# Performance work log

Hardware: AMD Instinct MI355X
Metric: run time of the kernel (lower is better)

Reference implementation:

```python
import jax, jax.numpy as jnp
import numpy as np

N_NODES = 250000
N_EDGES = 4000000
N_GRAPHS = 512
NEG_SLOPE = 0.01  # F.leaky_relu default


def _glorot(key, shape):
    fan_in, fan_out = shape
    lim = (6.0 / (fan_in + fan_out)) ** 0.5
    return jax.random.uniform(key, shape, jnp.float32, -lim, lim)


def setup_inputs() -> dict:
    key = jax.random.key(0)
    ks = jax.random.split(key, 12)
    x = jax.random.normal(ks[0], (N_NODES, 13), jnp.float32)
    edge_index = jax.random.randint(ks[1], (2, N_EDGES), 0, N_NODES, jnp.int64)
    batch_index = jnp.sort(jax.random.randint(ks[2], (N_NODES,), 0, N_GRAPHS, jnp.int64))
    # SAGEConv params: lin_l (neighbor agg, with bias), lin_r (self, no bias)
    dims = [(13, 16), (16, 8), (8, 4)]
    params = {}
    for i, (di, do) in enumerate(dims, 1):
        params[f'W{i}l'] = _glorot(ks[2 + 2 * i], (di, do))
        params[f'b{i}'] = jnp.zeros((do,), jnp.float32)
        params[f'W{i}r'] = _glorot(ks[3 + 2 * i], (di, do))
    params['Wc'] = _glorot(ks[10], (8, 1))
    params['bc'] = jnp.zeros((1,), jnp.float32)
    return dict(x=x, edge_index=edge_index, batch_index=batch_index, **params)


def _sage_conv(x, src, dst, Wl, bl, Wr):
    # mean-aggregate neighbor features at target nodes, then linear
    msg_sum = jax.ops.segment_sum(x[src], dst, num_segments=N_NODES)  # [N, d]
    cnt = jax.ops.segment_sum(jnp.ones((src.shape[0],), x.dtype), dst,
                              num_segments=N_NODES)
    agg = msg_sum / jnp.maximum(cnt, 1.0)[:, None]
    return agg @ Wl + bl + x @ Wr


def reference(x, edge_index, batch_index,
              W1l, b1, W1r, W2l, b2, W2r, W3l, b3, W3r, Wc, bc):
    src, dst = edge_index[0], edge_index[1]
    h = jax.nn.leaky_relu(_sage_conv(x, src, dst, W1l, b1, W1r), NEG_SLOPE)
    h = jax.nn.leaky_relu(_sage_conv(h, src, dst, W2l, b2, W2r), NEG_SLOPE)
    h = _sage_conv(h, src, dst, W3l, b3, W3r)  # [N, 4]
    add_pool = jax.ops.segment_sum(h, batch_index, num_segments=N_GRAPHS)  # [G,4]
    gcnt = jax.ops.segment_sum(jnp.ones((N_NODES,), h.dtype), batch_index,
                               num_segments=N_GRAPHS)
    mean_pool = add_pool / jnp.maximum(gcnt, 1.0)[:, None]
    g = jnp.concatenate([mean_pool, add_pool], axis=1)  # [G, 8]
    return g @ Wc + bc  # [G, 1]
```

## Files before the change

kernel.cpp:

```cpp
#include <hip/hip_runtime.h>

#define N_NODES 250000
#define N_EDGES 4000000
#define N_GRAPHS 512
#define NEG 0.01f
#define BINB 9
#define WIN 512
#define NBINS 489
#define NSUB (NBINS * 4)
#define CAPQ 2560
#define PART_EPB 8192
#define PART_BLOCKS 489
#define PACK_BLOCKS 1954

__device__ __forceinline__ float lrelu(float v) { return v > 0.0f ? v : NEG * v; }
__device__ __forceinline__ unsigned f2b(float f) {
    unsigned u = __float_as_uint(f);
    unsigned r = ((u >> 16) & 1u) + 0x7FFFu;
    return (u + r) >> 16;
}
__device__ __forceinline__ unsigned pk(float a, float b) { return f2b(a) | (f2b(b) << 16); }
__device__ __forceinline__ float blo(unsigned p) { return __uint_as_float(p << 16); }
__device__ __forceinline__ float bhi(unsigned p) { return __uint_as_float(p & 0xFFFF0000u); }

__global__ __launch_bounds__(1024) void part_pack_k(const int* __restrict__ src,
                                                    const int* __restrict__ dst,
                                                    int* __restrict__ qcnt,
                                                    unsigned* __restrict__ binned,
                                                    const float* __restrict__ x,
                                                    unsigned* __restrict__ x16b) {
    if (blockIdx.x >= PART_BLOCKS) {
        int tid = (blockIdx.x - PART_BLOCKS) * 1024 + threadIdx.x;
        if (tid < N_NODES * 8) {
            int n = tid >> 3, d2 = tid & 7;
            int a = d2 * 2, b = a + 1;
            float va = (a < 13) ? x[n * 13 + a] : 0.0f;
            float vb = (b < 13) ? x[n * 13 + b] : 0.0f;
            x16b[tid] = pk(va, vb);
        }
        return;
    }
    __shared__ int hist[NSUB];
    __shared__ int loff[NSUB];
    __shared__ int base[NSUB];
    __shared__ unsigned ebuf[PART_EPB];
    __shared__ unsigned short subid[PART_EPB];
    __shared__ int wsum[16];
    int t = threadIdx.x;
    for (int i = t; i < NSUB; i += 1024) hist[i] = 0;
    __syncthreads();
    unsigned e0 = blockIdx.x * PART_EPB;
    int m = min((int)PART_EPB, (int)(N_EDGES - e0));
    for (int i = t; i < m; i += 1024) {
        unsigned e = e0 + i;
        int s = ((dst[e] >> BINB) << 2) | (src[e] >> 16);
        atomicAdd(&hist[s], 1);
    }
    __syncthreads();
    int p = 0, s0 = 0, incl = 0;
    if (t < NSUB / 2) { s0 = hist[2 * t]; p = s0 + hist[2 * t + 1]; }
    incl = p;
#pragma unroll
    for (int d = 1; d < 64; d <<= 1) {
        int u = __shfl_up(incl, d, 64);
        if ((t & 63) >= d) incl += u;
    }
    if ((t & 63) == 63) wsum[t >> 6] = incl;
    __syncthreads();
    if (t == 0) {
        int r = 0;
#pragma unroll
        for (int i = 0; i < 16; i++) { int s = wsum[i]; wsum[i] = r; r += s; }
    }
    __syncthreads();
    if (t < NSUB / 2) {
        int ex = incl + wsum[t >> 6] - p;
        loff[2 * t] = ex;
        loff[2 * t + 1] = ex + s0;
    }
    __syncthreads();
    for (int i = t; i < NSUB; i += 1024) {
        int h = hist[i];
        base[i] = (h > 0) ? atomicAdd(&qcnt[i], h) : 0;
    }
    __syncthreads();
    for (int i = t; i < NSUB; i += 1024) hist[i] = loff[i];
    __syncthreads();
    for (int i = t; i < m; i += 1024) {
        unsigned e = e0 + i;
        int d = dst[e], sv = src[e];
        int s = ((d >> BINB) << 2) | (sv >> 16);
        int pos = atomicAdd(&hist[s], 1);
        ebuf[pos] = ((unsigned)(d & (WIN - 1)) << 18) | (unsigned)sv;
        subid[pos] = (unsigned short)s;
    }
    __syncthreads();
    for (int j = t; j < m; j += 1024) {
        int s = subid[j];
        binned[(size_t)s * CAPQ + base[s] + (j - loff[s])] = ebuf[j];
    }
}

__global__ __launch_bounds__(1024) void sortagg_k(const unsigned* __restrict__ x16b,
                                                  unsigned* __restrict__ binned,
                                                  const int* __restrict__ qcnt,
                                                  int* __restrict__ offs,
                                                  float* __restrict__ cntf,
                                                  float* __restrict__ agg) {
    __shared__ unsigned stg[CAPQ];
    __shared__ unsigned srt[CAPQ];
    __shared__ int hist[WIN];
    __shared__ int cur[WIN];
    __shared__ int wsum[8];
    int t = threadIdx.x;
    int bin = blockIdx.x;
    int f = t & (WIN - 1), l = t >> 9;
    int lane = t & 63, wv = t >> 6;
    float a0 = 0, a1 = 0, a2 = 0, a3 = 0, a4 = 0, a5 = 0, a6 = 0, a7 = 0;
    int deg = 0;
    for (int q = 0; q < 4; q++) {
        int sub = (bin << 2) | q;
        int cnt = qcnt[sub];
        unsigned* bp = binned + (size_t)sub * CAPQ;
        if (t < WIN) hist[t] = 0;
        __syncthreads();
        for (int i = t; i < cnt; i += 1024) {
            unsigned w = bp[i];
            stg[i] = w;
            atomicAdd(&hist[w >> 18], 1);
        }
        __syncthreads();
        int v = (t < WIN) ? hist[t] : 0;
#pragma unroll
        for (int d = 1; d < 64; d <<= 1) {
            int u = __shfl_up(v, d, 64);
            if (lane >= d) v += u;
        }
        if (t < WIN && lane == 63) wsum[wv] = v;
        __syncthreads();
        if (t == 0) {
            int r = 0;
#pragma unroll
            for (int i = 0; i < 8; i++) { int s = wsum[i]; wsum[i] = r; r += s; }
        }
        __syncthreads();
        if (t < WIN) {
            int incl = v + wsum[wv];
            int ex = incl - hist[t];
            cur[t] = ex;
            offs[(size_t)sub * 513 + t] = ex;
            deg += hist[t];
        }
        if (t == 0) offs[(size_t)sub * 513 + WIN] = cnt;
        __syncthreads();
        for (int i = t; i < cnt; i += 1024) {
            unsigned w = stg[i];
            int pos = atomicAdd(&cur[w >> 18], 1);
            srt[pos] = w;
        }
        __syncthreads();
        for (int i = t; i < cnt; i += 1024) bp[i] = srt[i];
        int e_ = cur[f];
        int s_ = e_ - hist[f];
        int k = s_;
        for (; k + 4 <= e_; k += 4) {
            unsigned w0 = srt[k], w1 = srt[k + 1], w2 = srt[k + 2], w3 = srt[k + 3];
            uint4 v0 = *(const uint4*)&x16b[(size_t)(w0 & 0x3FFFFu) * 8u + (unsigned)(l * 4)];
            uint4 v1 = *(const uint4*)&x16b[(size_t)(w1 & 0x3FFFFu) * 8u + (unsigned)(l * 4)];
            uint4 v2 = *(const uint4*)&x16b[(size_t)(w2 & 0x3FFFFu) * 8u + (unsigned)(l * 4)];
            uint4 v3 = *(const uint4*)&x16b[(size_t)(w3 & 0x3FFFFu) * 8u + (unsigned)(l * 4)];
            a0 += blo(v0.x) + blo(v1.x) + blo(v2.x) + blo(v3.x);
            a1 += bhi(v0.x) + bhi(v1.x) + bhi(v2.x) + bhi(v3.x);
            a2 += blo(v0.y) + blo(v1.y) + blo(v2.y) + blo(v3.y);
            a3 += bhi(v0.y) + bhi(v1.y) + bhi(v2.y) + bhi(v3.y);
            a4 += blo(v0.z) + blo(v1.z) + blo(v2.z) + blo(v3.z);
            a5 += bhi(v0.z) + bhi(v1.z) + bhi(v2.z) + bhi(v3.z);
            a6 += blo(v0.w) + blo(v1.w) + blo(v2.w) + blo(v3.w);
            a7 += bhi(v0.w) + bhi(v1.w) + bhi(v2.w) + bhi(v3.w);
        }
        for (; k < e_; k++) {
            unsigned w = srt[k];
            uint4 v4 = *(const uint4*)&x16b[(size_t)(w & 0x3FFFFu) * 8u + (unsigned)(l * 4)];
            a0 += blo(v4.x); a1 += bhi(v4.x); a2 += blo(v4.y); a3 += bhi(v4.y);
            a4 += blo(v4.z); a5 += bhi(v4.z); a6 += blo(v4.w); a7 += bhi(v4.w);
        }
        __syncthreads();
    }
    int g = (bin << BINB) + f;
    if (g < N_NODES) {
        size_t b = (size_t)g * 13;
        if (l == 0) {
            agg[b + 0] = a0; agg[b + 1] = a1; agg[b + 2] = a2; agg[b + 3] = a3;
            agg[b + 4] = a4; agg[b + 5] = a5; agg[b + 6] = a6; agg[b + 7] = a7;
            cntf[g] = (float)deg;
        } else {
            agg[b + 8] = a0; agg[b + 9] = a1; agg[b + 10] = a2;
            agg[b + 11] = a3; agg[b + 12] = a4;
        }
    }
}

__global__ __launch_bounds__(256) void fused1(const float* __restrict__ agg,
                                              const float* __restrict__ x,
                                              const float* __restrict__ cntf,
                                              const float* __restrict__ W1l,
                                              const float* __restrict__ b1,
                                              const float* __restrict__ W1r,
                                              const float* __restrict__ W2l,
                                              const float* __restrict__ W2r,
                                              unsigned* __restrict__ y2b,
                                              float* __restrict__ z2) {
    __shared__ float sWl[208], sWr[208], sb[16], sA[128], sB[128];
    for (int i = threadIdx.x; i < 208; i += blockDim.x) { sWl[i] = W1l[i]; sWr[i] = W1r[i]; }
    for (int i = threadIdx.x; i < 128; i += blockDim.x) { sA[i] = W2l[i]; sB[i] = W2r[i]; }
    if (threadIdx.x < 16) sb[threadIdx.x] = b1[threadIdx.x];
    __syncthreads();
    int n = blockIdx.x * blockDim.x + threadIdx.x;
    if (n >= N_NODES) return;
    float inv = 1.0f / fmaxf(cntf[n], 1.0f);
    float a[13], xv[13];
#pragma unroll
    for (int i = 0; i < 13; i++) { a[i] = agg[n * 13 + i] * inv; xv[i] = x[n * 13 + i]; }
    float h[16];
#pragma unroll
    for (int o = 0; o < 16; o++) {
        float acc = sb[o];
#pragma unroll
        for (int i = 0; i < 13; i++) acc += a[i] * sWl[i * 16 + o] + xv[i] * sWr[i * 16 + o];
        h[o] = lrelu(acc);
    }
    float ya[8];
#pragma unroll
    for (int o2 = 0; o2 < 8; o2++) {
        float y = 0.0f, za = 0.0f;
#pragma unroll
        for (int o = 0; o < 16; o++) { y += h[o] * sA[o * 8 + o2]; za += h[o] * sB[o * 8 + o2]; }
        ya[o2] = y;
        z2[n * 8 + o2] = za;
    }
    uint4 out;
    out.x = pk(ya[0], ya[1]); out.y = pk(ya[2], ya[3]);
    out.z = pk(ya[4], ya[5]); out.w = pk(ya[6], ya[7]);
    *(uint4*)&y2b[(size_t)n * 4u] = out;
}

__global__ __launch_bounds__(256) void agg8f_k(const unsigned* __restrict__ y2b,
                                               const unsigned* __restrict__ binned,
                                               const int* __restrict__ offs,
                                               const float* __restrict__ cntf,
                                               const float* __restrict__ b2,
                                               const float* __restrict__ W3l,
                                               float* __restrict__ z2h2,
                                               unsigned* __restrict__ y3b,
                                               float* __restrict__ pool) {
    __shared__ float sb[8], sW3[32];
    if (blockIdx.x == 0) {
        for (int i = threadIdx.x; i < N_GRAPHS * 5; i += 256) pool[i] = 0.0f;
    }
    if (threadIdx.x < 8) sb[threadIdx.x] = b2[threadIdx.x];
    if (threadIdx.x < 32) sW3[threadIdx.x] = W3l[threadIdx.x];
    __syncthreads();
    int g = blockIdx.x * 256 + threadIdx.x;
    if (g >= N_NODES) return;
    int bin = g >> BINB, f = g & (WIN - 1);
    float a0 = 0, a1 = 0, a2 = 0, a3 = 0, a4 = 0, a5 = 0, a6 = 0, a7 = 0;
#pragma unroll
    for (int q = 0; q < 4; q++) {
        int sub = (bin << 2) | q;
        const int* o = offs + (size_t)sub * 513;
        int s = o[f], e = o[f + 1];
        const unsigned* bp = binned + (size_t)sub * CAPQ;
        int k = s;
        for (; k + 4 <= e; k += 4) {
            unsigned w0 = bp[k], w1 = bp[k + 1], w2 = bp[k + 2], w3 = bp[k + 3];
            uint4 v0 = *(const uint4*)&y2b[(size_t)(w0 & 0x3FFFFu) * 4u];
            uint4 v1 = *(const uint4*)&y2b[(size_t)(w1 & 0x3FFFFu) * 4u];
            uint4 v2 = *(const uint4*)&y2b[(size_t)(w2 & 0x3FFFFu) * 4u];
            uint4 v3 = *(const uint4*)&y2b[(size_t)(w3 & 0x3FFFFu) * 4u];
            a0 += blo(v0.x) + blo(v1.x) + blo(v2.x) + blo(v3.x);
            a1 += bhi(v0.x) + bhi(v1.x) + bhi(v2.x) + bhi(v3.x);
            a2 += blo(v0.y) + blo(v1.y) + blo(v2.y) + blo(v3.y);
            a3 += bhi(v0.y) + bhi(v1.y) + bhi(v2.y) + bhi(v3.y);
            a4 += blo(v0.z) + blo(v1.z) + blo(v2.z) + blo(v3.z);
            a5 += bhi(v0.z) + bhi(v1.z) + bhi(v2.z) + bhi(v3.z);
            a6 += blo(v0.w) + blo(v1.w) + blo(v2.w) + blo(v3.w);
            a7 += bhi(v0.w) + bhi(v1.w) + bhi(v2.w) + bhi(v3.w);
        }
        for (; k < e; k++) {
            uint4 v = *(const uint4*)&y2b[(size_t)(bp[k] & 0x3FFFFu) * 4u];
            a0 += blo(v.x); a1 += bhi(v.x); a2 += blo(v.y); a3 += bhi(v.y);
            a4 += blo(v.z); a5 += bhi(v.z); a6 += blo(v.w); a7 += bhi(v.w);
        }
    }
    float inv = 1.0f / fmaxf(cntf[g], 1.0f);
    float h2v[8];
    float s8[8] = {a0, a1, a2, a3, a4, a5, a6, a7};
#pragma unroll
    for (int j = 0; j < 8; j++) {
        float v = s8[j] * inv + sb[j] + z2h2[(size_t)g * 8 + j];
        h2v[j] = lrelu(v);
        z2h2[(size_t)g * 8 + j] = h2v[j];
    }
    float y[4];
#pragma unroll
    for (int k = 0; k < 4; k++) {
        float acc = 0.0f;
#pragma unroll
        for (int j = 0; j < 8; j++) acc += h2v[j] * sW3[j * 4 + k];
        y[k] = acc;
    }
    uint2 out;
    out.x = pk(y[0], y[1]); out.y = pk(y[2], y[3]);
    *(uint2*)&y3b[(size_t)g * 2u] = out;
}

__global__ __launch_bounds__(256) void agg4pool_k(const unsigned* __restrict__ y3b,
                                                  const unsigned* __restrict__ binned,
                                                  const int* __restrict__ offs,
                                                  const float* __restrict__ cntf,
                                                  const float* __restrict__ h2,
                                                  const float* __restrict__ W3r,
                                                  const float* __restrict__ b3,
                                                  const int* __restrict__ batch,
                                                  float* __restrict__ pool,
                                                  float* __restrict__ gcnt) {
    __shared__ float sW[32], sb[4];
    __shared__ float lp[16][4];
    __shared__ float lc[16];
    __shared__ int sbase;
    if (threadIdx.x < 32) sW[threadIdx.x] = W3r[threadIdx.x];
    if (threadIdx.x < 4) sb[threadIdx.x] = b3[threadIdx.x];
    if (threadIdx.x < 16) {
        lc[threadIdx.x] = 0.0f;
        for (int k = 0; k < 4; k++) lp[threadIdx.x][k] = 0.0f;
    }
    int n0 = blockIdx.x * 256;
    if (threadIdx.x == 0) sbase = batch[n0 < N_NODES ? n0 : N_NODES - 1];
    __syncthreads();
    int g = n0 + threadIdx.x;
    if (g < N_NODES) {
        int bin = g >> BINB, f = g & (WIN - 1);
        float a0 = 0, a1 = 0, a2 = 0, a3 = 0;
#pragma unroll
        for (int q = 0; q < 4; q++) {
            int sub = (bin << 2) | q;
            const int* o = offs + (size_t)sub * 513;
            int s = o[f], e = o[f + 1];
            const unsigned* bp = binned + (size_t)sub * CAPQ;
            int k = s;
            for (; k + 4 <= e; k += 4) {
                unsigned w0 = bp[k], w1 = bp[k + 1], w2 = bp[k + 2], w3 = bp[k + 3];
                uint2 v0 = *(const uint2*)&y3b[(size_t)(w0 & 0x3FFFFu) * 2u];
                uint2 v1 = *(const uint2*)&y3b[(size_t)(w1 & 0x3FFFFu) * 2u];
                uint2 v2 = *(const uint2*)&y3b[(size_t)(w2 & 0x3FFFFu) * 2u];
                uint2 v3 = *(const uint2*)&y3b[(size_t)(w3 & 0x3FFFFu) * 2u];
                a0 += blo(v0.x) + blo(v1.x) + blo(v2.x) + blo(v3.x);
                a1 += bhi(v0.x) + bhi(v1.x) + bhi(v2.x) + bhi(v3.x);
                a2 += blo(v0.y) + blo(v1.y) + blo(v2.y) + blo(v3.y);
                a3 += bhi(v0.y) + bhi(v1.y) + bhi(v2.y) + bhi(v3.y);
            }
            for (; k < e; k++) {
                uint2 v = *(const uint2*)&y3b[(size_t)(bp[k] & 0x3FFFFu) * 2u];
                a0 += blo(v.x); a1 += bhi(v.x); a2 += blo(v.y); a3 += bhi(v.y);
            }
        }
        float inv = 1.0f / fmaxf(cntf[g], 1.0f);
        float s4[4] = {a0, a1, a2, a3};
        float h2v[8];
#pragma unroll
        for (int j = 0; j < 8; j++) h2v[j] = h2[(size_t)g * 8 + j];
        int b = batch[g];
        int off = b - sbase;
        bool local = (off >= 0 && off < 16);
#pragma unroll
        for (int k = 0; k < 4; k++) {
            float z = 0.0f;
#pragma unroll
            for (int j = 0; j < 8; j++) z += h2v[j] * sW[j * 4 + k];
            float v = s4[k] * inv + sb[k] + z;
            if (local) atomicAdd(&lp[off][k], v);
            else atomicAdd(&pool[b * 4 + k], v);
        }
        if (local) atomicAdd(&lc[off], 1.0f);
        else atomicAdd(&gcnt[b], 1.0f);
    }
    __syncthreads();
    if (threadIdx.x < 16) {
        int b = sbase + threadIdx.x;
        float c = lc[threadIdx.x];
        if (c > 0.0f && b < N_GRAPHS) {
            atomicAdd(&gcnt[b], c);
            for (int k = 0; k < 4; k++) atomicAdd(&pool[b * 4 + k], lp[threadIdx.x][k]);
        }
    }
}

__global__ __launch_bounds__(256) void final_k(const float* __restrict__ pool,
                                               const float* __restrict__ gcnt,
                                               const float* __restrict__ Wc,
                                               const float* __restrict__ bc,
                                               float* __restrict__ out) {
    int g = blockIdx.x * blockDim.x + threadIdx.x;
    if (g >= N_GRAPHS) return;
    float inv = 1.0f / fmaxf(gcnt[g], 1.0f);
    float acc = bc[0];
#pragma unroll
    for (int k = 0; k < 4; k++) {
        float ap = pool[g * 4 + k];
        acc += ap * inv * Wc[k] + ap * Wc[4 + k];
    }
    out[g] = acc;
}

extern "C" void kernel_launch(void* const* d_in, const int* in_sizes, int n_in,
                              void* d_out, int out_size, void* d_ws, size_t ws_size,
                              hipStream_t stream) {
    const float* x = (const float*)d_in[0];
    const int* ei = (const int*)d_in[1];
    const int* src = ei;
    const int* dst = ei + N_EDGES;
    const int* batch = (const int*)d_in[2];
    const float* W1l = (const float*)d_in[3];
    const float* b1 = (const float*)d_in[4];
    const float* W1r = (const float*)d_in[5];
    const float* W2l = (const float*)d_in[6];
    const float* b2 = (const float*)d_in[7];
    const float* W2r = (const float*)d_in[8];
    const float* W3l = (const float*)d_in[9];
    const float* b3 = (const float*)d_in[10];
    const float* W3r = (const float*)d_in[11];
    const float* Wc = (const float*)d_in[12];
    const float* bc = (const float*)d_in[13];
    float* out = (float*)d_out;

    const size_t N = N_NODES;
    unsigned* binned = (unsigned*)d_ws;
    int* qcnt = (int*)(binned + (size_t)NSUB * CAPQ);
    int* offs = qcnt + 2048;
    float* fbase = (float*)(offs + (size_t)NSUB * 513);
    float* agg = fbase;
    float* cntf = fbase + 13 * N;
    float* z2 = cntf + N;
    unsigned* x16b = (unsigned*)(z2 + 8 * N);
    unsigned* y2b = x16b + 8 * N;
    unsigned* y3b = y2b + 4 * N;
    float* pool = (float*)(y3b + 2 * N);
    float* gcnt = pool + N_GRAPHS * 4;

    const int TPB = 256;
    const int NB = (N_NODES + TPB - 1) / TPB;

    hipMemsetAsync(qcnt, 0, NSUB * sizeof(int), stream);
    part_pack_k<<<PART_BLOCKS + PACK_BLOCKS, 1024, 0, stream>>>(src, dst, qcnt, binned, x, x16b);
    sortagg_k<<<NBINS, 1024, 0, stream>>>(x16b, binned, qcnt, offs, cntf, agg);
    fused1<<<NB, TPB, 0, stream>>>(agg, x, cntf, W1l, b1, W1r, W2l, W2r, y2b, z2);
    agg8f_k<<<NB, TPB, 0, stream>>>(y2b, binned, offs, cntf, b2, W3l, z2, y3b, pool);
    agg4pool_k<<<NB, TPB, 0, stream>>>(y3b, binned, offs, cntf, z2, W3r, b3, batch, pool, gcnt);
    final_k<<<2, TPB, 0, stream>>>(pool, gcnt, Wc, bc, out);
}
```

Measured before the change: 271.2 us.

## Store sorted edge lists as 16-bit sources and cache edges in registers during partition

The partition kernel now loads each edge's src/dst once into registers and reuses them for both the histogram and the scatter pass, where it previously read them from global memory twice. The sort kernel writes the sorted edge list as 16-bit low source bits into a separate buffer, and the two later aggregation kernels rebuild the full source index from the sub-bin number. This halves the index bytes read by the second and third layers' gathers. The cost is extra register pressure in a 1024-thread block and a new workspace region placed after the existing buffers.

```diff
diff --git a/kernel.cpp b/kernel.cpp
--- a/kernel.cpp
+++ b/kernel.cpp
@@ -10,6 +10,7 @@
 #define NSUB (NBINS * 4)
 #define CAPQ 2560
 #define PART_EPB 8192
+#define EPT 8
 #define PART_BLOCKS 489
 #define PACK_BLOCKS 1954
 
@@ -51,10 +52,20 @@
     __syncthreads();
     unsigned e0 = blockIdx.x * PART_EPB;
     int m = min((int)PART_EPB, (int)(N_EDGES - e0));
-    for (int i = t; i < m; i += 1024) {
-        unsigned e = e0 + i;
-        int s = ((dst[e] >> BINB) << 2) | (src[e] >> 16);
-        atomicAdd(&hist[s], 1);
+    int sreg[EPT];
+    unsigned wreg[EPT];
+#pragma unroll
+    for (int j = 0; j < EPT; j++) {
+        int i = t + j * 1024;
+        sreg[j] = -1;
+        if (i < m) {
+            unsigned e = e0 + i;
+            int d = dst[e], sv = src[e];
+            int s = ((d >> BINB) << 2) | (sv >> 16);
+            sreg[j] = s;
+            wreg[j] = ((unsigned)(d & (WIN - 1)) << 18) | (unsigned)sv;
+            atomicAdd(&hist[s], 1);
+        }
     }
     __syncthreads();
     int p = 0, s0 = 0, incl = 0;
@@ -86,13 +97,13 @@
     __syncthreads();
     for (int i = t; i < NSUB; i += 1024) hist[i] = loff[i];
     __syncthreads();
-    for (int i = t; i < m; i += 1024) {
-        unsigned e = e0 + i;
-        int d = dst[e], sv = src[e];
-        int s = ((d >> BINB) << 2) | (sv >> 16);
-        int pos = atomicAdd(&hist[s], 1);
-        ebuf[pos] = ((unsigned)(d & (WIN - 1)) << 18) | (unsigned)sv;
-        subid[pos] = (unsigned short)s;
+#pragma unroll
+    for (int j = 0; j < EPT; j++) {
+        if (sreg[j] >= 0) {
+            int pos = atomicAdd(&hist[sreg[j]], 1);
+            ebuf[pos] = wreg[j];
+            subid[pos] = (unsigned short)sreg[j];
+        }
     }
     __syncthreads();
     for (int j = t; j < m; j += 1024) {
@@ -102,7 +113,8 @@
 }
 
 __global__ __launch_bounds__(1024) void sortagg_k(const unsigned* __restrict__ x16b,
-                                                  unsigned* __restrict__ binned,
+                                                  const unsigned* __restrict__ binned,
+                                                  unsigned short* __restrict__ binned16,
                                                   const int* __restrict__ qcnt,
                                                   int* __restrict__ offs,
                                                   float* __restrict__ cntf,
@@ -121,7 +133,8 @@
     for (int q = 0; q < 4; q++) {
         int sub = (bin << 2) | q;
         int cnt = qcnt[sub];
-        unsigned* bp = binned + (size_t)sub * CAPQ;
+        const unsigned* bp = binned + (size_t)sub * CAPQ;
+        unsigned short* bp16 = binned16 + (size_t)sub * CAPQ;
         if (t < WIN) hist[t] = 0;
         __syncthreads();
         for (int i = t; i < cnt; i += 1024) {
@@ -159,7 +172,7 @@
             srt[pos] = w;
         }
         __syncthreads();
-        for (int i = t; i < cnt; i += 1024) bp[i] = srt[i];
+        for (int i = t; i < cnt; i += 1024) bp16[i] = (unsigned short)srt[i];
         int e_ = cur[f];
         int s_ = e_ - hist[f];
         int k = s_;
@@ -245,7 +258,7 @@
 }
 
 __global__ __launch_bounds__(256) void agg8f_k(const unsigned* __restrict__ y2b,
-                                               const unsigned* __restrict__ binned,
+                                               const unsigned short* __restrict__ binned16,
                                                const int* __restrict__ offs,
                                                const float* __restrict__ cntf,
                                                const float* __restrict__ b2,
@@ -269,14 +282,16 @@
         int sub = (bin << 2) | q;
         const int* o = offs + (size_t)sub * 513;
         int s = o[f], e = o[f + 1];
-        const unsigned* bp = binned + (size_t)sub * CAPQ;
+        const unsigned short* bp = binned16 + (size_t)sub * CAPQ;
+        unsigned qb = (unsigned)q << 16;
         int k = s;
         for (; k + 4 <= e; k += 4) {
-            unsigned w0 = bp[k], w1 = bp[k + 1], w2 = bp[k + 2], w3 = bp[k + 3];
-            uint4 v0 = *(const uint4*)&y2b[(size_t)(w0 & 0x3FFFFu) * 4u];
-            uint4 v1 = *(const uint4*)&y2b[(size_t)(w1 & 0x3FFFFu) * 4u];
-            uint4 v2 = *(const uint4*)&y2b[(size_t)(w2 & 0x3FFFFu) * 4u];
-            uint4 v3 = *(const uint4*)&y2b[(size_t)(w3 & 0x3FFFFu) * 4u];
+            unsigned w0 = qb | bp[k], w1 = qb | bp[k + 1];
+            unsigned w2 = qb | bp[k + 2], w3 = qb | bp[k + 3];
+            uint4 v0 = *(const uint4*)&y2b[(size_t)w0 * 4u];
+            uint4 v1 = *(const uint4*)&y2b[(size_t)w1 * 4u];
+            uint4 v2 = *(const uint4*)&y2b[(size_t)w2 * 4u];
+            uint4 v3 = *(const uint4*)&y2b[(size_t)w3 * 4u];
             a0 += blo(v0.x) + blo(v1.x) + blo(v2.x) + blo(v3.x);
             a1 += bhi(v0.x) + bhi(v1.x) + bhi(v2.x) + bhi(v3.x);
             a2 += blo(v0.y) + blo(v1.y) + blo(v2.y) + blo(v3.y);
@@ -287,7 +302,7 @@
             a7 += bhi(v0.w) + bhi(v1.w) + bhi(v2.w) + bhi(v3.w);
         }
         for (; k < e; k++) {
-            uint4 v = *(const uint4*)&y2b[(size_t)(bp[k] & 0x3FFFFu) * 4u];
+            uint4 v = *(const uint4*)&y2b[(size_t)(qb | bp[k]) * 4u];
             a0 += blo(v.x); a1 += bhi(v.x); a2 += blo(v.y); a3 += bhi(v.y);
             a4 += blo(v.z); a5 += bhi(v.z); a6 += blo(v.w); a7 += bhi(v.w);
         }
@@ -315,7 +330,7 @@
 }
 
 __global__ __launch_bounds__(256) void agg4pool_k(const unsigned* __restrict__ y3b,
-                                                  const unsigned* __restrict__ binned,
+                                                  const unsigned short* __restrict__ binned16,
                                                   const int* __restrict__ offs,
                                                   const float* __restrict__ cntf,
                                                   const float* __restrict__ h2,
@@ -346,21 +361,23 @@
             int sub = (bin << 2) | q;
             const int* o = offs + (size_t)sub * 513;
             int s = o[f], e = o[f + 1];
-            const unsigned* bp = binned + (size_t)sub * CAPQ;
+            const unsigned short* bp = binned16 + (size_t)sub * CAPQ;
+            unsigned qb = (unsigned)q << 16;
             int k = s;
             for (; k + 4 <= e; k += 4) {
-                unsigned w0 = bp[k], w1 = bp[k + 1], w2 = bp[k + 2], w3 = bp[k + 3];
-                uint2 v0 = *(const uint2*)&y3b[(size_t)(w0 & 0x3FFFFu) * 2u];
-                uint2 v1 = *(const uint2*)&y3b[(size_t)(w1 & 0x3FFFFu) * 2u];
-                uint2 v2 = *(const uint2*)&y3b[(size_t)(w2 & 0x3FFFFu) * 2u];
-                uint2 v3 = *(const uint2*)&y3b[(size_t)(w3 & 0x3FFFFu) * 2u];
+                unsigned w0 = qb | bp[k], w1 = qb | bp[k + 1];
+                unsigned w2 = qb | bp[k + 2], w3 = qb | bp[k + 3];
+                uint2 v0 = *(const uint2*)&y3b[(size_t)w0 * 2u];
+                uint2 v1 = *(const uint2*)&y3b[(size_t)w1 * 2u];
+                uint2 v2 = *(const uint2*)&y3b[(size_t)w2 * 2u];
+                uint2 v3 = *(const uint2*)&y3b[(size_t)w3 * 2u];
                 a0 += blo(v0.x) + blo(v1.x) + blo(v2.x) + blo(v3.x);
                 a1 += bhi(v0.x) + bhi(v1.x) + bhi(v2.x) + bhi(v3.x);
                 a2 += blo(v0.y) + blo(v1.y) + blo(v2.y) + blo(v3.y);
                 a3 += bhi(v0.y) + bhi(v1.y) + bhi(v2.y) + bhi(v3.y);
             }
             for (; k < e; k++) {
-                uint2 v = *(const uint2*)&y3b[(size_t)(bp[k] & 0x3FFFFu) * 2u];
+                uint2 v = *(const uint2*)&y3b[(size_t)(qb | bp[k]) * 2u];
                 a0 += blo(v.x); a1 += bhi(v.x); a2 += blo(v.y); a3 += bhi(v.y);
             }
         }
@@ -446,15 +463,16 @@
     unsigned* y3b = y2b + 4 * N;
     float* pool = (float*)(y3b + 2 * N);
     float* gcnt = pool + N_GRAPHS * 4;
+    unsigned short* binned16 = (unsigned short*)(gcnt + N_GRAPHS);
 
     const int TPB = 256;
     const int NB = (N_NODES + TPB - 1) / TPB;
 
     hipMemsetAsync(qcnt, 0, NSUB * sizeof(int), stream);
     part_pack_k<<<PART_BLOCKS + PACK_BLOCKS, 1024, 0, stream>>>(src, dst, qcnt, binned, x, x16b);
-    sortagg_k<<<NBINS, 1024, 0, stream>>>(x16b, binned, qcnt, offs, cntf, agg);
+    sortagg_k<<<NBINS, 1024, 0, stream>>>(x16b, binned, binned16, qcnt, offs, cntf, agg);
     fused1<<<NB, TPB, 0, stream>>>(agg, x, cntf, W1l, b1, W1r, W2l, W2r, y2b, z2);
-    agg8f_k<<<NB, TPB, 0, stream>>>(y2b, binned, offs, cntf, b2, W3l, z2, y3b, pool);
-    agg4pool_k<<<NB, TPB, 0, stream>>>(y3b, binned, offs, cntf, z2, W3r, b3, batch, pool, gcnt);
+    agg8f_k<<<NB, TPB, 0, stream>>>(y2b, binned16, offs, cntf, b2, W3l, z2, y3b, pool);
+    agg4pool_k<<<NB, TPB, 0, stream>>>(y3b, binned16, offs, cntf, z2, W3r, b3, batch, pool, gcnt);
     final_k<<<2, TPB, 0, stream>>>(pool, gcnt, Wc, bc, out);
 }
```

New measurement: 279.2 us. +3.0%, slower.
